# Kernel optimization log

Measured on AMD Instinct MI355X. Metric: run time of the kernel, lower is better.

The kernel has to match this reference:

```python
import jax, jax.numpy as jnp
import numpy as np
from jax import lax

SIGMA = 1.0
NUM_ITER = 6
NEG = -1e4  # log-domain 'impossible' (fp16-safe)
S = 4       # trellis states (memory-2 RSC)

# RSC code, generators (7,5) octal: feedback 1+D+D^2, feedforward 1+D^2.
# state s = 2*s1 + s2 (s1 = newest register).
_NS = np.zeros((S, 2), np.int32)   # next state per (state, input bit)
_PAR = np.zeros((S, 2), np.int32)  # parity bit per (state, input bit)
for _s in range(S):
    _s1, _s2 = _s >> 1, _s & 1
    for _u in (0, 1):
        _a = _u ^ _s1 ^ _s2          # feedback bit
        _NS[_s, _u] = (_a << 1) | _s1
        _PAR[_s, _u] = _a ^ _s2
NS = jnp.asarray(_NS)                      # [S,2]
NS_FLAT = jnp.asarray(_NS.reshape(-1))     # [S*2], branch i = s*2+u
PAR_FLAT = jnp.asarray(_PAR.reshape(-1))
PAR_BPSK = jnp.asarray(2.0 * _PAR - 1.0, jnp.float32)  # [S,2]
U_BPSK = jnp.asarray([-1.0, 1.0], jnp.float32)


def rsc_encode(bits):
    # bits: [B,K] int32 -> parity bits [B,K] int32 (trellis scan from state 0)
    B = bits.shape[0]
    def step(state, u):
        idx = state * 2 + u
        return NS_FLAT[idx], PAR_FLAT[idx]
    _, p = lax.scan(step, jnp.zeros((B,), jnp.int32), bits.T)
    return p.T


def bcjr(y_sys, y_par, La, Lc):
    # max-log-MAP BCJR. y_sys, y_par, La: [B,T] -> full LLR [B,T]
    B, T = y_sys.shape
    # branch metrics gamma[b,t,s,u]
    gamma = 0.5 * ((Lc * y_sys + La)[:, :, None, None] * U_BPSK
                   + (Lc * y_par)[:, :, None, None] * PAR_BPSK)  # [B,T,S,2]
    gamma_t = jnp.moveaxis(gamma, 1, 0)  # [T,B,S,2]

    # forward recursion (alpha), start in state 0
    alpha0 = jnp.full((B, S), NEG, y_sys.dtype).at[:, 0].set(0.0)
    def fwd(alpha, g):
        cand = (alpha[:, :, None] + g).reshape(B, S * 2)          # [B,8]
        new = jax.ops.segment_max(cand.T, NS_FLAT, num_segments=S).T  # [B,S]
        new = new - new.max(axis=1, keepdims=True)
        return new, alpha                                          # emit alpha_t (pre-step)
    _, alphas = lax.scan(fwd, alpha0, gamma_t)                     # [T,B,S]

    # backward recursion (beta), unterminated trellis -> uniform end
    beta_end = jnp.zeros((B, S), y_sys.dtype)
    def bwd(beta, g):
        new = (g + beta[:, NS]).max(axis=2)                        # [B,S]
        new = new - new.max(axis=1, keepdims=True)
        return new, beta                                           # emit beta_{t+1}
    _, betas = lax.scan(bwd, beta_end, gamma_t, reverse=True)      # [T,B,S]

    metric = alphas[:, :, :, None] + gamma_t + betas[:, :, NS]     # [T,B,S,2]
    llr = metric[..., 1].max(axis=2) - metric[..., 0].max(axis=2)  # [T,B]
    return llr.T


def _turbo(x, n1, n2, n3, interleaver):
    # encode: rate-1/3 turbo (systematic + 2 RSC parities), BPSK, AWGN
    c1 = 2.0 * x.astype(jnp.float32) - 1.0
    c2 = 2.0 * rsc_encode(x).astype(jnp.float32) - 1.0
    xi = jnp.take(x, interleaver, axis=1)
    c3 = 2.0 * rsc_encode(xi).astype(jnp.float32) - 1.0
    y1 = c1 + SIGMA * n1
    y2 = c2 + SIGMA * n2
    y1i = jnp.take(y1, interleaver, axis=1)
    y3 = c3 + SIGMA * n3

    inv = jnp.argsort(interleaver)
    Lc = 2.0 / (SIGMA * SIGMA)
    L_int = jnp.zeros_like(y1)
    L2 = L_int
    for _ in range(NUM_ITER):
        L1 = bcjr(y1, y2, L_int, Lc)
        Le1 = L1 - Lc * y1 - L_int            # extrinsic of decoder 1
        Le1_i = jnp.take(Le1, interleaver, axis=1)
        L2 = bcjr(y1i, y3, Le1_i, Lc)
        Le2 = L2 - Lc * y1i - Le1_i           # extrinsic of decoder 2
        L_int = jnp.take(Le2, inv, axis=1)    # deinterleave
    return jnp.take(L2, inv, axis=1)          # final deinterleaved LLR logits [B,K]


def setup_inputs() -> dict:
    key = jax.random.key(0)
    k1, k2, k3, k4, k5 = jax.random.split(key, 5)
    B, K = 512, 2048
    x = jax.random.randint(k1, (B, K), 0, 2).astype(jnp.int32)
    n1 = jax.random.normal(k2, (B, K), jnp.float32)
    n2 = jax.random.normal(k3, (B, K), jnp.float32)
    n3 = jax.random.normal(k4, (B, K), jnp.float32)
    interleaver = jax.random.permutation(k5, K).astype(jnp.int32)
    return {"x": x, "n1": n1, "n2": n2, "n3": n3, "interleaver": interleaver}


def reference(x, n1, n2, n3, interleaver):
    return _turbo(x, n1, n2, n3, interleaver)
```

## Files before the change

kernel.cpp:

```cpp
#include <hip/hip_runtime.h>

#define KLEN 2048
#define SCH 8
#define TPR 256
#define NEGV (-1e4f)

struct SM {
  float y1[KLEN];
  float y1i[KLEN];
  float Lint[KLEN];
  float A[KLEN];
  unsigned short perm[KLEN];
  unsigned short invp[KLEN];
  float fT[4][16];
  float bT[4][16];
  unsigned int eT[4][2];
};

template <int CTRL>
__device__ __forceinline__ float dppf(float src) {
  return __int_as_float(__builtin_amdgcn_update_dpp(
      __float_as_int(src), __float_as_int(src), CTRL, 0xF, 0xF, false));
}

template <int CTRL>
__device__ __forceinline__ void shift16(const float (&X)[16], float (&T)[16]) {
#pragma unroll
  for (int e = 0; e < 16; ++e) T[e] = dppf<CTRL>(X[e]);
}

__device__ __forceinline__ void cp16(float (&D)[16], const float (&S)[16]) {
#pragma unroll
  for (int e = 0; e < 16; ++e) D[e] = S[e];
}

__device__ __forceinline__ void ld16(float (&D)[16], const float* S) {
#pragma unroll
  for (int e = 0; e < 16; ++e) D[e] = S[e];
}

__device__ __forceinline__ void comb(const float (&X)[16], const float (&Y)[16],
                                     float (&Z)[16]) {
#pragma unroll
  for (int i = 0; i < 4; ++i)
#pragma unroll
    for (int j = 0; j < 4; ++j)
      Z[i * 4 + j] = fmaxf(fmaxf(X[i * 4 + 0] + Y[0 * 4 + j], X[i * 4 + 1] + Y[1 * 4 + j]),
                           fmaxf(X[i * 4 + 2] + Y[2 * 4 + j], X[i * 4 + 3] + Y[3 * 4 + j]));
}

__device__ __forceinline__ void buildM(const float (&p)[SCH], const float (&q)[SCH],
                                       float (&M)[16]) {
  float ppq = p[0] + q[0], pmq = p[0] - q[0];
  M[0] = -ppq; M[1] =  ppq; M[2] = NEGV; M[3] = NEGV;
  M[4] = NEGV; M[5] = NEGV; M[6] =  pmq; M[7] = -pmq;
  M[8] =  ppq; M[9] = -ppq; M[10] = NEGV; M[11] = NEGV;
  M[12] = NEGV; M[13] = NEGV; M[14] = -pmq; M[15] =  pmq;
#pragma unroll
  for (int k = 1; k < SCH; ++k) {
    ppq = p[k] + q[k]; pmq = p[k] - q[k];
#pragma unroll
    for (int j = 0; j < 4; ++j) {
      float r0 = M[0 * 4 + j], r1 = M[1 * 4 + j], r2 = M[2 * 4 + j], r3 = M[3 * 4 + j];
      M[0 * 4 + j] = fmaxf(r0 - ppq, r1 + ppq);
      M[2 * 4 + j] = fmaxf(r0 + ppq, r1 - ppq);
      M[1 * 4 + j] = fmaxf(r2 + pmq, r3 - pmq);
      M[3 * 4 + j] = fmaxf(r2 - pmq, r3 + pmq);
    }
  }
  float mx = M[0];
#pragma unroll
  for (int e = 1; e < 16; ++e) mx = fmaxf(mx, M[e]);
#pragma unroll
  for (int e = 0; e < 16; ++e) M[e] -= mx;
}

__device__ __forceinline__ void bcjr_pass(
    const float* ys, const float* La, float* dst, const unsigned short* widx,
    int finalLLR, const float (&q)[SCH], float (&fT)[4][16], float (&bT)[4][16],
    int c, int lane, int w) {
  const int base = c * SCH;
  float p[SCH];
  {
    const float4* y4 = (const float4*)(ys + base);
    const float4* l4 = (const float4*)(La + base);
#pragma unroll
    for (int k = 0; k < SCH / 4; ++k) {
      float4 yv = y4[k], lv = l4[k];
      p[4 * k + 0] = yv.x + 0.5f * lv.x;
      p[4 * k + 1] = yv.y + 0.5f * lv.y;
      p[4 * k + 2] = yv.z + 0.5f * lv.z;
      p[4 * k + 3] = yv.w + 0.5f * lv.w;
    }
  }

  float P[16];
  buildM(p, q, P);
  float Q[16];
  cp16(Q, P);

  const int rl = lane & 15;
  const int row = lane >> 4;

  {
    float T[16], N[16];
    shift16<0x111>(P, T); if (rl >= 1) { comb(P, T, N); cp16(P, N); }
    shift16<0x112>(P, T); if (rl >= 2) { comb(P, T, N); cp16(P, N); }
    shift16<0x114>(P, T); if (rl >= 4) { comb(P, T, N); cp16(P, N); }
    shift16<0x118>(P, T); if (rl >= 8) { comb(P, T, N); cp16(P, N); }
    shift16<0x142>(P, T); if (row & 1)  { comb(P, T, N); cp16(P, N); }
    shift16<0x143>(P, T); if (row >= 2) { comb(P, T, N); cp16(P, N); }
  }
  {
    float T[16], N[16];
    shift16<0x101>(Q, T); if (rl <= 14) { comb(T, Q, N); cp16(Q, N); }
    shift16<0x102>(Q, T); if (rl <= 13) { comb(T, Q, N); cp16(Q, N); }
    shift16<0x104>(Q, T); if (rl <= 11) { comb(T, Q, N); cp16(Q, N); }
    shift16<0x108>(Q, T); if (rl <= 7)  { comb(T, Q, N); cp16(Q, N); }
#pragma unroll
    for (int d = 1; d <= 2; d <<= 1) {
      int src = (row + d) << 4;
      float T2[16];
#pragma unroll
      for (int e = 0; e < 16; ++e) T2[e] = __shfl(Q[e], src);
      if (row + d <= 3) { float N2[16]; comb(T2, Q, N2); cp16(Q, N2); }
    }
  }

  if (lane == 63) {
#pragma unroll
    for (int e = 0; e < 16; ++e) fT[w][e] = P[e];
  }
  if (lane == 0) {
#pragma unroll
    for (int e = 0; e < 16; ++e) bT[w][e] = Q[e];
  }
  __syncthreads();

  float F[16];
  {
    float t[16], n[16];
    if (w >= 1) ld16(F, fT[0]);
    if (w >= 2) { ld16(t, fT[1]); comb(t, F, n); cp16(F, n); }
    if (w >= 3) { ld16(t, fT[2]); comb(t, F, n); cp16(F, n); }
    if (w >= 1) { comb(P, F, n); cp16(P, n); }
  }
  float Bm[16];
  {
    float t[16], n[16];
    if (w <= 2) ld16(Bm, bT[3]);
    if (w <= 1) { ld16(t, bT[2]); comb(Bm, t, n); cp16(Bm, n); }
    if (w <= 0) { ld16(t, bT[1]); comb(Bm, t, n); cp16(Bm, n); }
    if (w <= 2) { comb(Bm, Q, n); cp16(Q, n); }
  }

  float a[4];
  {
    float a0 = __shfl(P[0], lane - 1), a1 = __shfl(P[4], lane - 1);
    float a2 = __shfl(P[8], lane - 1), a3 = __shfl(P[12], lane - 1);
    if (c == 0) { a[0] = 0.f; a[1] = NEGV; a[2] = NEGV; a[3] = NEGV; }
    else {
      if (lane == 0) { a0 = F[0]; a1 = F[4]; a2 = F[8]; a3 = F[12]; }
      a[0] = 0.f; a[1] = a1 - a0; a[2] = a2 - a0; a[3] = a3 - a0;
    }
  }

  float b[4];
  {
    float m0 = fmaxf(fmaxf(Q[0], Q[4]), fmaxf(Q[8],  Q[12]));
    float m1 = fmaxf(fmaxf(Q[1], Q[5]), fmaxf(Q[9],  Q[13]));
    float m2 = fmaxf(fmaxf(Q[2], Q[6]), fmaxf(Q[10], Q[14]));
    float m3 = fmaxf(fmaxf(Q[3], Q[7]), fmaxf(Q[11], Q[15]));
    float b0 = __shfl(m0, lane + 1), b1 = __shfl(m1, lane + 1);
    float b2 = __shfl(m2, lane + 1), b3 = __shfl(m3, lane + 1);
    if (c == TPR - 1) { b[0] = b[1] = b[2] = b[3] = 0.f; }
    else {
      if (lane == 63) {
        b0 = fmaxf(fmaxf(Bm[0], Bm[4]), fmaxf(Bm[8],  Bm[12]));
        b1 = fmaxf(fmaxf(Bm[1], Bm[5]), fmaxf(Bm[9],  Bm[13]));
        b2 = fmaxf(fmaxf(Bm[2], Bm[6]), fmaxf(Bm[10], Bm[14]));
        b3 = fmaxf(fmaxf(Bm[3], Bm[7]), fmaxf(Bm[11], Bm[15]));
      }
      b[0] = 0.f; b[1] = b1 - b0; b[2] = b2 - b0; b[3] = b3 - b0;
    }
  }

  float bet[SCH][4];
  bet[SCH - 1][0] = b[0]; bet[SCH - 1][1] = b[1];
  bet[SCH - 1][2] = b[2]; bet[SCH - 1][3] = b[3];
#pragma unroll
  for (int k = SCH - 1; k >= 1; --k) {
    float ppq = p[k] + q[k], pmq = p[k] - q[k];
    float B0 = bet[k][0], B1 = bet[k][1], B2 = bet[k][2], B3 = bet[k][3];
    bet[k - 1][0] = fmaxf(B0 - ppq, B2 + ppq);
    bet[k - 1][1] = fmaxf(B2 - ppq, B0 + ppq);
    bet[k - 1][2] = fmaxf(B3 - pmq, B1 + pmq);
    bet[k - 1][3] = fmaxf(B1 - pmq, B3 + pmq);
  }

#pragma unroll
  for (int k = 0; k < SCH; ++k) {
    float ppq = p[k] + q[k], pmq = p[k] - q[k];
    float B0 = bet[k][0], B1 = bet[k][1], B2 = bet[k][2], B3 = bet[k][3];
    float m1 = fmaxf(fmaxf(a[0] + ppq + B2, a[1] + ppq + B0),
                     fmaxf(a[2] + pmq + B1, a[3] + pmq + B3));
    float m0 = fmaxf(fmaxf(a[0] - ppq + B0, a[1] - ppq + B2),
                     fmaxf(a[2] - pmq + B3, a[3] - pmq + B1));
    float llr = m1 - m0;
    float val = finalLLR ? llr : (llr - 2.f * p[k]);
    dst[widx[base + k]] = val;
    float a0 = a[0], a1 = a[1], a2 = a[2], a3 = a[3];
    a[0] = fmaxf(a0 - ppq, a1 + ppq);
    a[2] = fmaxf(a0 + ppq, a1 - ppq);
    a[1] = fmaxf(a2 + pmq, a3 - pmq);
    a[3] = fmaxf(a2 - pmq, a3 + pmq);
  }
}

__device__ __forceinline__ unsigned fsm_compose(unsigned f, unsigned g) {
  unsigned nm = 0;
#pragma unroll
  for (int s = 0; s < 4; ++s) {
    unsigned gs = (g >> (8 * s)) & 3u;
    nm |= ((f >> (8 * gs)) & 0xFFu) << (8 * s);
  }
  return nm;
}

__global__ __launch_bounds__(TPR, 2) void turbo_kernel(
    const int* __restrict__ xg, const float* __restrict__ n1g,
    const float* __restrict__ n2g, const float* __restrict__ n3g,
    const int* __restrict__ pg, float* __restrict__ outg) {
  __shared__ SM sm;
  const int tid = threadIdx.x;
  const int c = tid, lane = tid & 63, w = tid >> 6;
  const size_t rb = (size_t)blockIdx.x * KLEN;

  int* Ai = (int*)sm.A;
  for (int i = tid; i < KLEN; i += TPR) {
    sm.perm[i] = (unsigned short)pg[i];
    int xv = xg[rb + i];
    Ai[i] = xv;
    sm.y1[i] = (2.f * xv - 1.f) + n1g[rb + i];
    sm.Lint[i] = 0.f;
  }
  float q2[SCH], q3[SCH];
  {
    size_t g0 = rb + (size_t)c * SCH;
#pragma unroll
    for (int k = 0; k < SCH; ++k) { q2[k] = n2g[g0 + k]; q3[k] = n3g[g0 + k]; }
  }
  __syncthreads();

  for (int i = tid; i < KLEN; i += TPR) {
    sm.invp[sm.perm[i]] = (unsigned short)i;
    sm.y1i[i] = sm.y1[sm.perm[i]];
  }

  unsigned ub1 = 0, ub2 = 0;
#pragma unroll
  for (int k = 0; k < SCH; ++k) {
    int t = c * SCH + k;
    ub1 |= (unsigned)(Ai[t] & 1) << k;
    ub2 |= (unsigned)(Ai[sm.perm[t]] & 1) << k;
  }
  unsigned m1 = 0x03020100u, m2 = 0x03020100u;
#pragma unroll
  for (int k = 0; k < SCH; ++k) {
    unsigned st1 = ((ub1 >> k) & 1) ? 0x03010002u : 0x01030200u;
    unsigned st2 = ((ub2 >> k) & 1) ? 0x03010002u : 0x01030200u;
    m1 = fsm_compose(st1, m1);
    m2 = fsm_compose(st2, m2);
  }
#pragma unroll
  for (int i = 0; i < 6; ++i) {
    const int d = 1 << i;
    unsigned t1 = __shfl_up(m1, d), t2 = __shfl_up(m2, d);
    if (lane >= d) { m1 = fsm_compose(m1, t1); m2 = fsm_compose(m2, t2); }
  }
  if (lane == 63) { sm.eT[w][0] = m1; sm.eT[w][1] = m2; }
  __syncthreads();
  {
    unsigned W1 = 0x03020100u, W2 = 0x03020100u;
    if (w >= 1) { W1 = sm.eT[0][0]; W2 = sm.eT[0][1]; }
    if (w >= 2) { W1 = fsm_compose(sm.eT[1][0], W1); W2 = fsm_compose(sm.eT[1][1], W2); }
    if (w >= 3) { W1 = fsm_compose(sm.eT[2][0], W1); W2 = fsm_compose(sm.eT[2][1], W2); }
    unsigned f1 = fsm_compose(m1, W1), f2 = fsm_compose(m2, W2);
    unsigned pf1 = __shfl_up(f1, 1), pf2 = __shfl_up(f2, 1);
    int s1 = (c == 0) ? 0 : (lane == 0 ? (int)(W1 & 3u) : (int)(pf1 & 3u));
    int s2 = (c == 0) ? 0 : (lane == 0 ? (int)(W2 & 3u) : (int)(pf2 & 3u));
#pragma unroll
    for (int k = 0; k < SCH; ++k) {
      { int u = (ub1 >> k) & 1, a = u ^ (s1 >> 1) ^ (s1 & 1), par = a ^ (s1 & 1);
        q2[k] += 2.f * par - 1.f; s1 = (a << 1) | (s1 >> 1); }
      { int u = (ub2 >> k) & 1, a = u ^ (s2 >> 1) ^ (s2 & 1), par = a ^ (s2 & 1);
        q3[k] += 2.f * par - 1.f; s2 = (a << 1) | (s2 >> 1); }
    }
  }
  __syncthreads();

#pragma unroll 1
  for (int it = 0; it < 6; ++it) {
    bcjr_pass(sm.y1, sm.Lint, sm.A, sm.invp, 0, q2, sm.fT, sm.bT, c, lane, w);
    __syncthreads();
    const int fin = (it == 5);
    bcjr_pass(sm.y1i, sm.A, sm.Lint, sm.perm, fin, q3, sm.fT, sm.bT, c, lane, w);
    __syncthreads();
  }

  for (int i = tid; i < KLEN; i += TPR) outg[rb + i] = sm.Lint[i];
}

extern "C" void kernel_launch(void* const* d_in, const int* in_sizes, int n_in,
                              void* d_out, int out_size, void* d_ws, size_t ws_size,
                              hipStream_t stream) {
  (void)n_in; (void)d_ws; (void)ws_size; (void)out_size;
  const int* x    = (const int*)d_in[0];
  const float* n1 = (const float*)d_in[1];
  const float* n2 = (const float*)d_in[2];
  const float* n3 = (const float*)d_in[3];
  const int* perm = (const int*)d_in[4];
  float* out = (float*)d_out;
  const int K = in_sizes[4];
  const int B = in_sizes[0] / K;
  turbo_kernel<<<B, TPR, 0, stream>>>(x, n1, n2, n3, perm, out);
}
```

Baseline: 174.7 us.

## Use packed fp32 adds with reordered 4x4 matrix layout in BCJR scans

Reorders the 4x4 max-plus transition matrices and the alpha/beta state vectors into pairs of float2 and computes the additions with inline-asm v_pk_add_f32 using op_sel broadcasts. The goal is to roughly halve the VALU add instructions in the parallel prefix combines, in matrix construction and in the per-step alpha/beta recursions. The max operations stay scalar, and the inline asm may constrain register allocation and scheduling. DPP and shuffle counts are unchanged.

```diff
diff --git a/kernel.cpp b/kernel.cpp
--- a/kernel.cpp
+++ b/kernel.cpp
@@ -4,6 +4,24 @@
 #define SCH 8
 #define TPR 256
 #define NEGV (-1e4f)
+
+typedef float v2f __attribute__((ext_vector_type(2)));
+
+static __device__ __forceinline__ v2f pka(v2f a, v2f b) {
+  v2f d; asm("v_pk_add_f32 %0, %1, %2" : "=v"(d) : "v"(a), "v"(b)); return d;
+}
+static __device__ __forceinline__ v2f pkabl(v2f a, v2f b) {
+  v2f d; asm("v_pk_add_f32 %0, %1, %2 op_sel:[0,0] op_sel_hi:[1,0]"
+             : "=v"(d) : "v"(a), "v"(b)); return d;
+}
+static __device__ __forceinline__ v2f pkabh(v2f a, v2f b) {
+  v2f d; asm("v_pk_add_f32 %0, %1, %2 op_sel:[0,1] op_sel_hi:[1,1]"
+             : "=v"(d) : "v"(a), "v"(b)); return d;
+}
+static __device__ __forceinline__ v2f pkasw(v2f a, v2f b) {
+  v2f d; asm("v_pk_add_f32 %0, %1, %2 op_sel:[0,1] op_sel_hi:[1,0]"
+             : "=v"(d) : "v"(a), "v"(b)); return d;
+}
 
 struct SM {
   float y1[KLEN];
@@ -12,72 +30,89 @@
   float A[KLEN];
   unsigned short perm[KLEN];
   unsigned short invp[KLEN];
-  float fT[4][16];
-  float bT[4][16];
+  v2f fT[4][8];
+  v2f bT[4][8];
   unsigned int eT[4][2];
 };
 
+
 template <int CTRL>
-__device__ __forceinline__ float dppf(float src) {
-  return __int_as_float(__builtin_amdgcn_update_dpp(
-      __float_as_int(src), __float_as_int(src), CTRL, 0xF, 0xF, false));
+__device__ __forceinline__ v2f dpp2(v2f x) {
+  int lo = __builtin_amdgcn_update_dpp(__float_as_int(x.x), __float_as_int(x.x),
+                                       CTRL, 0xF, 0xF, false);
+  int hi = __builtin_amdgcn_update_dpp(__float_as_int(x.y), __float_as_int(x.y),
+                                       CTRL, 0xF, 0xF, false);
+  v2f r; r.x = __int_as_float(lo); r.y = __int_as_float(hi); return r;
 }
 
 template <int CTRL>
-__device__ __forceinline__ void shift16(const float (&X)[16], float (&T)[16]) {
-#pragma unroll
-  for (int e = 0; e < 16; ++e) T[e] = dppf<CTRL>(X[e]);
-}
-
-__device__ __forceinline__ void cp16(float (&D)[16], const float (&S)[16]) {
-#pragma unroll
-  for (int e = 0; e < 16; ++e) D[e] = S[e];
-}
-
-__device__ __forceinline__ void ld16(float (&D)[16], const float* S) {
-#pragma unroll
-  for (int e = 0; e < 16; ++e) D[e] = S[e];
-}
-
-__device__ __forceinline__ void comb(const float (&X)[16], const float (&Y)[16],
-                                     float (&Z)[16]) {
-#pragma unroll
-  for (int i = 0; i < 4; ++i)
-#pragma unroll
-    for (int j = 0; j < 4; ++j)
-      Z[i * 4 + j] = fmaxf(fmaxf(X[i * 4 + 0] + Y[0 * 4 + j], X[i * 4 + 1] + Y[1 * 4 + j]),
-                           fmaxf(X[i * 4 + 2] + Y[2 * 4 + j], X[i * 4 + 3] + Y[3 * 4 + j]));
+__device__ __forceinline__ void shift8(const v2f (&X)[8], v2f (&T)[8]) {
+#pragma unroll
+  for (int e = 0; e < 8; ++e) T[e] = dpp2<CTRL>(X[e]);
+}
+
+__device__ __forceinline__ void cp8(v2f (&D)[8], const v2f (&S)[8]) {
+#pragma unroll
+  for (int e = 0; e < 8; ++e) D[e] = S[e];
+}
+
+__device__ __forceinline__ void comb(const v2f (&X)[8], const v2f (&Y)[8],
+                                     v2f (&Z)[8]) {
+#pragma unroll
+  for (int j = 0; j < 4; ++j) {
+    v2f y01 = Y[2 * j], y23 = Y[2 * j + 1];
+    v2f a0 = pkabl(X[0], y01), b0 = pkabl(X[1], y01);
+    v2f a1 = pkabh(X[2], y01), b1 = pkabh(X[3], y01);
+    v2f a2 = pkabl(X[4], y23), b2 = pkabl(X[5], y23);
+    v2f a3 = pkabh(X[6], y23), b3 = pkabh(X[7], y23);
+    v2f z01, z23;
+    z01.x = fmaxf(fmaxf(a0.x, a1.x), fmaxf(a2.x, a3.x));
+    z01.y = fmaxf(fmaxf(a0.y, a1.y), fmaxf(a2.y, a3.y));
+    z23.x = fmaxf(fmaxf(b0.x, b1.x), fmaxf(b2.x, b3.x));
+    z23.y = fmaxf(fmaxf(b0.y, b1.y), fmaxf(b2.y, b3.y));
+    Z[2 * j] = z01; Z[2 * j + 1] = z23;
+  }
 }
 
 __device__ __forceinline__ void buildM(const float (&p)[SCH], const float (&q)[SCH],
-                                       float (&M)[16]) {
-  float ppq = p[0] + q[0], pmq = p[0] - q[0];
-  M[0] = -ppq; M[1] =  ppq; M[2] = NEGV; M[3] = NEGV;
-  M[4] = NEGV; M[5] = NEGV; M[6] =  pmq; M[7] = -pmq;
-  M[8] =  ppq; M[9] = -ppq; M[10] = NEGV; M[11] = NEGV;
-  M[12] = NEGV; M[13] = NEGV; M[14] = -pmq; M[15] =  pmq;
+                                       v2f (&X)[8]) {
+  {
+    float ppq = p[0] + q[0], pmq = p[0] - q[0];
+    X[0].x = -ppq; X[0].y = NEGV;  X[1].x =  ppq; X[1].y = NEGV;
+    X[2].x =  ppq; X[2].y = NEGV;  X[3].x = -ppq; X[3].y = NEGV;
+    X[4].x = NEGV; X[4].y =  pmq;  X[5].x = NEGV; X[5].y = -pmq;
+    X[6].x = NEGV; X[6].y = -pmq;  X[7].x = NEGV; X[7].y =  pmq;
+  }
 #pragma unroll
   for (int k = 1; k < SCH; ++k) {
-    ppq = p[k] + q[k]; pmq = p[k] - q[k];
+    float ppq = p[k] + q[k], pmq = p[k] - q[k];
+    v2f Wp; Wp.x = -ppq; Wp.y = ppq;
+    v2f Wm; Wm.x = pmq;  Wm.y = -pmq;
 #pragma unroll
     for (int j = 0; j < 4; ++j) {
-      float r0 = M[0 * 4 + j], r1 = M[1 * 4 + j], r2 = M[2 * 4 + j], r3 = M[3 * 4 + j];
-      M[0 * 4 + j] = fmaxf(r0 - ppq, r1 + ppq);
-      M[2 * 4 + j] = fmaxf(r0 + ppq, r1 - ppq);
-      M[1 * 4 + j] = fmaxf(r2 + pmq, r3 - pmq);
-      M[3 * 4 + j] = fmaxf(r2 - pmq, r3 + pmq);
-    }
-  }
-  float mx = M[0];
-#pragma unroll
-  for (int e = 1; e < 16; ++e) mx = fmaxf(mx, M[e]);
-#pragma unroll
-  for (int e = 0; e < 16; ++e) M[e] -= mx;
+      v2f c01 = X[2 * j], c23 = X[2 * j + 1];
+      v2f t = pka(c01, Wp);
+      v2f u = pkasw(c01, Wp);
+      v2f v = pka(c23, Wm);
+      v2f s = pkasw(c23, Wm);
+      v2f n01, n23;
+      n01.x = fmaxf(t.x, t.y); n01.y = fmaxf(v.x, v.y);
+      n23.x = fmaxf(u.x, u.y); n23.y = fmaxf(s.x, s.y);
+      X[2 * j] = n01; X[2 * j + 1] = n23;
+    }
+  }
+  float mx = fmaxf(fmaxf(fmaxf(X[0].x, X[0].y), fmaxf(X[1].x, X[1].y)),
+                   fmaxf(fmaxf(X[2].x, X[2].y), fmaxf(X[3].x, X[3].y)));
+  mx = fmaxf(mx, fmaxf(fmaxf(fmaxf(X[4].x, X[4].y), fmaxf(X[5].x, X[5].y)),
+                       fmaxf(fmaxf(X[6].x, X[6].y), fmaxf(X[7].x, X[7].y))));
+  v2f mn; mn.x = -mx; mn.y = -mx;
+#pragma unroll
+  for (int e = 0; e < 8; ++e) X[e] = pka(X[e], mn);
 }
 
 __device__ __forceinline__ void bcjr_pass(
     const float* ys, const float* La, float* dst, const unsigned short* widx,
-    int finalLLR, const float (&q)[SCH], float (&fT)[4][16], float (&bT)[4][16],
+    int finalLLR, const float (&q)[SCH], v2f (&fT)[4][8], v2f (&bT)[4][8],
     int c, int lane, int w) {
   const int base = c * SCH;
   float p[SCH];
@@ -94,126 +129,129 @@
     }
   }
 
-  float P[16];
+  v2f P[8];
   buildM(p, q, P);
-  float Q[16];
-  cp16(Q, P);
+  v2f Q[8];
+  cp8(Q, P);
 
   const int rl = lane & 15;
   const int row = lane >> 4;
 
   {
-    float T[16], N[16];
-    shift16<0x111>(P, T); if (rl >= 1) { comb(P, T, N); cp16(P, N); }
-    shift16<0x112>(P, T); if (rl >= 2) { comb(P, T, N); cp16(P, N); }
-    shift16<0x114>(P, T); if (rl >= 4) { comb(P, T, N); cp16(P, N); }
-    shift16<0x118>(P, T); if (rl >= 8) { comb(P, T, N); cp16(P, N); }
-    shift16<0x142>(P, T); if (row & 1)  { comb(P, T, N); cp16(P, N); }
-    shift16<0x143>(P, T); if (row >= 2) { comb(P, T, N); cp16(P, N); }
-  }
-  {
-    float T[16], N[16];
-    shift16<0x101>(Q, T); if (rl <= 14) { comb(T, Q, N); cp16(Q, N); }
-    shift16<0x102>(Q, T); if (rl <= 13) { comb(T, Q, N); cp16(Q, N); }
-    shift16<0x104>(Q, T); if (rl <= 11) { comb(T, Q, N); cp16(Q, N); }
-    shift16<0x108>(Q, T); if (rl <= 7)  { comb(T, Q, N); cp16(Q, N); }
+    v2f T[8], N[8];
+    shift8<0x111>(P, T); if (rl >= 1) { comb(P, T, N); cp8(P, N); }
+    shift8<0x112>(P, T); if (rl >= 2) { comb(P, T, N); cp8(P, N); }
+    shift8<0x114>(P, T); if (rl >= 4) { comb(P, T, N); cp8(P, N); }
+    shift8<0x118>(P, T); if (rl >= 8) { comb(P, T, N); cp8(P, N); }
+    shift8<0x142>(P, T); if (row & 1)  { comb(P, T, N); cp8(P, N); }
+    shift8<0x143>(P, T); if (row >= 2) { comb(P, T, N); cp8(P, N); }
+  }
+  {
+    v2f T[8], N[8];
+    shift8<0x101>(Q, T); if (rl <= 14) { comb(T, Q, N); cp8(Q, N); }
+    shift8<0x102>(Q, T); if (rl <= 13) { comb(T, Q, N); cp8(Q, N); }
+    shift8<0x104>(Q, T); if (rl <= 11) { comb(T, Q, N); cp8(Q, N); }
+    shift8<0x108>(Q, T); if (rl <= 7)  { comb(T, Q, N); cp8(Q, N); }
 #pragma unroll
     for (int d = 1; d <= 2; d <<= 1) {
       int src = (row + d) << 4;
-      float T2[16];
-#pragma unroll
-      for (int e = 0; e < 16; ++e) T2[e] = __shfl(Q[e], src);
-      if (row + d <= 3) { float N2[16]; comb(T2, Q, N2); cp16(Q, N2); }
-    }
-  }
-
-  if (lane == 63) {
-#pragma unroll
-    for (int e = 0; e < 16; ++e) fT[w][e] = P[e];
-  }
-  if (lane == 0) {
-#pragma unroll
-    for (int e = 0; e < 16; ++e) bT[w][e] = Q[e];
-  }
+      v2f T2[8];
+#pragma unroll
+      for (int e = 0; e < 8; ++e) {
+        T2[e].x = __shfl(Q[e].x, src);
+        T2[e].y = __shfl(Q[e].y, src);
+      }
+      if (row + d <= 3) { v2f N2[8]; comb(T2, Q, N2); cp8(Q, N2); }
+    }
+  }
+
+  if (lane == 63) cp8(fT[w], P);
+  if (lane == 0)  cp8(bT[w], Q);
   __syncthreads();
 
-  float F[16];
-  {
-    float t[16], n[16];
-    if (w >= 1) ld16(F, fT[0]);
-    if (w >= 2) { ld16(t, fT[1]); comb(t, F, n); cp16(F, n); }
-    if (w >= 3) { ld16(t, fT[2]); comb(t, F, n); cp16(F, n); }
-    if (w >= 1) { comb(P, F, n); cp16(P, n); }
-  }
-  float Bm[16];
-  {
-    float t[16], n[16];
-    if (w <= 2) ld16(Bm, bT[3]);
-    if (w <= 1) { ld16(t, bT[2]); comb(Bm, t, n); cp16(Bm, n); }
-    if (w <= 0) { ld16(t, bT[1]); comb(Bm, t, n); cp16(Bm, n); }
-    if (w <= 2) { comb(Bm, Q, n); cp16(Q, n); }
-  }
-
-  float a[4];
-  {
-    float a0 = __shfl(P[0], lane - 1), a1 = __shfl(P[4], lane - 1);
-    float a2 = __shfl(P[8], lane - 1), a3 = __shfl(P[12], lane - 1);
-    if (c == 0) { a[0] = 0.f; a[1] = NEGV; a[2] = NEGV; a[3] = NEGV; }
+  v2f F[8];
+  {
+    v2f t[8], n[8];
+    if (w >= 1) cp8(F, fT[0]);
+    if (w >= 2) { cp8(t, fT[1]); comb(t, F, n); cp8(F, n); }
+    if (w >= 3) { cp8(t, fT[2]); comb(t, F, n); cp8(F, n); }
+    if (w >= 1) { comb(P, F, n); cp8(P, n); }
+  }
+  v2f Bm[8];
+  {
+    v2f t[8], n[8];
+    if (w <= 2) cp8(Bm, bT[3]);
+    if (w <= 1) { cp8(t, bT[2]); comb(Bm, t, n); cp8(Bm, n); }
+    if (w <= 0) { cp8(t, bT[1]); comb(Bm, t, n); cp8(Bm, n); }
+    if (w <= 2) { comb(Bm, Q, n); cp8(Q, n); }
+  }
+
+  v2f A01, A23;
+  {
+    float a0 = __shfl(P[0].x, lane - 1), a1 = __shfl(P[0].y, lane - 1);
+    float a2 = __shfl(P[1].x, lane - 1), a3 = __shfl(P[1].y, lane - 1);
+    if (c == 0) { A01.x = 0.f; A01.y = NEGV; A23.x = NEGV; A23.y = NEGV; }
     else {
-      if (lane == 0) { a0 = F[0]; a1 = F[4]; a2 = F[8]; a3 = F[12]; }
-      a[0] = 0.f; a[1] = a1 - a0; a[2] = a2 - a0; a[3] = a3 - a0;
-    }
-  }
-
-  float b[4];
-  {
-    float m0 = fmaxf(fmaxf(Q[0], Q[4]), fmaxf(Q[8],  Q[12]));
-    float m1 = fmaxf(fmaxf(Q[1], Q[5]), fmaxf(Q[9],  Q[13]));
-    float m2 = fmaxf(fmaxf(Q[2], Q[6]), fmaxf(Q[10], Q[14]));
-    float m3 = fmaxf(fmaxf(Q[3], Q[7]), fmaxf(Q[11], Q[15]));
+      if (lane == 0) { a0 = F[0].x; a1 = F[0].y; a2 = F[1].x; a3 = F[1].y; }
+      A01.x = 0.f; A01.y = a1 - a0; A23.x = a2 - a0; A23.y = a3 - a0;
+    }
+  }
+
+  v2f B02, B13;
+  {
+    float m0 = fmaxf(fmaxf(Q[0].x, Q[0].y), fmaxf(Q[1].x, Q[1].y));
+    float m1 = fmaxf(fmaxf(Q[2].x, Q[2].y), fmaxf(Q[3].x, Q[3].y));
+    float m2 = fmaxf(fmaxf(Q[4].x, Q[4].y), fmaxf(Q[5].x, Q[5].y));
+    float m3 = fmaxf(fmaxf(Q[6].x, Q[6].y), fmaxf(Q[7].x, Q[7].y));
     float b0 = __shfl(m0, lane + 1), b1 = __shfl(m1, lane + 1);
     float b2 = __shfl(m2, lane + 1), b3 = __shfl(m3, lane + 1);
-    if (c == TPR - 1) { b[0] = b[1] = b[2] = b[3] = 0.f; }
+    if (c == TPR - 1) { B02.x = 0.f; B02.y = 0.f; B13.x = 0.f; B13.y = 0.f; }
     else {
       if (lane == 63) {
-        b0 = fmaxf(fmaxf(Bm[0], Bm[4]), fmaxf(Bm[8],  Bm[12]));
-        b1 = fmaxf(fmaxf(Bm[1], Bm[5]), fmaxf(Bm[9],  Bm[13]));
-        b2 = fmaxf(fmaxf(Bm[2], Bm[6]), fmaxf(Bm[10], Bm[14]));
-        b3 = fmaxf(fmaxf(Bm[3], Bm[7]), fmaxf(Bm[11], Bm[15]));
+        b0 = fmaxf(fmaxf(Bm[0].x, Bm[0].y), fmaxf(Bm[1].x, Bm[1].y));
+        b1 = fmaxf(fmaxf(Bm[2].x, Bm[2].y), fmaxf(Bm[3].x, Bm[3].y));
+        b2 = fmaxf(fmaxf(Bm[4].x, Bm[4].y), fmaxf(Bm[5].x, Bm[5].y));
+        b3 = fmaxf(fmaxf(Bm[6].x, Bm[6].y), fmaxf(Bm[7].x, Bm[7].y));
       }
-      b[0] = 0.f; b[1] = b1 - b0; b[2] = b2 - b0; b[3] = b3 - b0;
-    }
-  }
-
-  float bet[SCH][4];
-  bet[SCH - 1][0] = b[0]; bet[SCH - 1][1] = b[1];
-  bet[SCH - 1][2] = b[2]; bet[SCH - 1][3] = b[3];
+      B02.x = 0.f; B02.y = b2 - b0; B13.x = b1 - b0; B13.y = b3 - b0;
+    }
+  }
+
+  v2f bet02[SCH], bet13[SCH];
+  bet02[SCH - 1] = B02; bet13[SCH - 1] = B13;
 #pragma unroll
   for (int k = SCH - 1; k >= 1; --k) {
     float ppq = p[k] + q[k], pmq = p[k] - q[k];
-    float B0 = bet[k][0], B1 = bet[k][1], B2 = bet[k][2], B3 = bet[k][3];
-    bet[k - 1][0] = fmaxf(B0 - ppq, B2 + ppq);
-    bet[k - 1][1] = fmaxf(B2 - ppq, B0 + ppq);
-    bet[k - 1][2] = fmaxf(B3 - pmq, B1 + pmq);
-    bet[k - 1][3] = fmaxf(B1 - pmq, B3 + pmq);
+    v2f Wp; Wp.x = -ppq; Wp.y = ppq;
+    v2f Wm; Wm.x = pmq;  Wm.y = -pmq;
+    v2f P02 = bet02[k], P13 = bet13[k];
+    v2f t = pka(P02, Wp);
+    v2f u = pkasw(P02, Wp);
+    v2f v = pka(P13, Wm);
+    v2f s = pkasw(P13, Wm);
+    v2f n02, n13;
+    n02.x = fmaxf(t.x, t.y);  n02.y = fmaxf(v.x, v.y);
+    n13.x = fmaxf(u.x, u.y);  n13.y = fmaxf(s.x, s.y);
+    bet02[k - 1] = n02; bet13[k - 1] = n13;
   }
 
 #pragma unroll
   for (int k = 0; k < SCH; ++k) {
     float ppq = p[k] + q[k], pmq = p[k] - q[k];
-    float B0 = bet[k][0], B1 = bet[k][1], B2 = bet[k][2], B3 = bet[k][3];
-    float m1 = fmaxf(fmaxf(a[0] + ppq + B2, a[1] + ppq + B0),
-                     fmaxf(a[2] + pmq + B1, a[3] + pmq + B3));
-    float m0 = fmaxf(fmaxf(a[0] - ppq + B0, a[1] - ppq + B2),
-                     fmaxf(a[2] - pmq + B3, a[3] - pmq + B1));
+    v2f Wp; Wp.x = -ppq; Wp.y = ppq;
+    v2f Wm; Wm.x = pmq;  Wm.y = -pmq;
+    v2f t = pka(A01, Wp);
+    v2f u = pkasw(A01, Wp);
+    v2f v = pka(A23, Wm);
+    v2f s = pkasw(A23, Wm);
+    float B0 = bet02[k].x, B2 = bet02[k].y, B1 = bet13[k].x, B3 = bet13[k].y;
+    float m1 = fmaxf(fmaxf(t.y + B0, u.x + B2), fmaxf(v.x + B1, s.y + B3));
+    float m0 = fmaxf(fmaxf(t.x + B0, u.y + B2), fmaxf(s.x + B3, v.y + B1));
     float llr = m1 - m0;
     float val = finalLLR ? llr : (llr - 2.f * p[k]);
     dst[widx[base + k]] = val;
-    float a0 = a[0], a1 = a[1], a2 = a[2], a3 = a[3];
-    a[0] = fmaxf(a0 - ppq, a1 + ppq);
-    a[2] = fmaxf(a0 + ppq, a1 - ppq);
-    a[1] = fmaxf(a2 + pmq, a3 - pmq);
-    a[3] = fmaxf(a2 - pmq, a3 + pmq);
+    A01.x = fmaxf(t.x, t.y);  A01.y = fmaxf(v.x, v.y);
+    A23.x = fmaxf(u.x, u.y);  A23.y = fmaxf(s.x, s.y);
   }
 }
 
```

Measured after the change: 202.0 us. +15.7%, slower.

## Replace matrix-matrix cross-wave combines with vector-matrix products in BCJR scan

Applied to the files above, without the earlier changes.

Forward and backward boundary states are now propagated as 4-element vectors times 4x4 max-plus matrices instead of full 16-element matrix-matrix compositions. The backward suffix across waves reuses the forward total matrices stored in shared memory, so the separate backward shared table and its write are dropped. The two cross-row shuffle-combine steps on Q are replaced by vector-matrix updates. This cuts max-plus arithmetic, register pressure and LDS traffic per pass, at the cost of three serial row shuffles of 16 values each.

```diff
diff --git a/kernel.cpp b/kernel.cpp
--- a/kernel.cpp
+++ b/kernel.cpp
@@ -13,7 +13,6 @@
   unsigned short perm[KLEN];
   unsigned short invp[KLEN];
   float fT[4][16];
-  float bT[4][16];
   unsigned int eT[4][2];
 };
 
@@ -34,11 +33,6 @@
   for (int e = 0; e < 16; ++e) D[e] = S[e];
 }
 
-__device__ __forceinline__ void ld16(float (&D)[16], const float* S) {
-#pragma unroll
-  for (int e = 0; e < 16; ++e) D[e] = S[e];
-}
-
 __device__ __forceinline__ void comb(const float (&X)[16], const float (&Y)[16],
                                      float (&Z)[16]) {
 #pragma unroll
@@ -47,6 +41,22 @@
     for (int j = 0; j < 4; ++j)
       Z[i * 4 + j] = fmaxf(fmaxf(X[i * 4 + 0] + Y[0 * 4 + j], X[i * 4 + 1] + Y[1 * 4 + j]),
                            fmaxf(X[i * 4 + 2] + Y[2 * 4 + j], X[i * 4 + 3] + Y[3 * 4 + j]));
+}
+
+__device__ __forceinline__ void matcol(const float* T, float (&f)[4]) {
+  float r0 = fmaxf(fmaxf(T[0]  + f[0], T[1]  + f[1]), fmaxf(T[2]  + f[2], T[3]  + f[3]));
+  float r1 = fmaxf(fmaxf(T[4]  + f[0], T[5]  + f[1]), fmaxf(T[6]  + f[2], T[7]  + f[3]));
+  float r2 = fmaxf(fmaxf(T[8]  + f[0], T[9]  + f[1]), fmaxf(T[10] + f[2], T[11] + f[3]));
+  float r3 = fmaxf(fmaxf(T[12] + f[0], T[13] + f[1]), fmaxf(T[14] + f[2], T[15] + f[3]));
+  f[0] = r0; f[1] = r1; f[2] = r2; f[3] = r3;
+}
+
+__device__ __forceinline__ void rowmat(float (&u)[4], const float* T) {
+  float c0 = fmaxf(fmaxf(u[0] + T[0], u[1] + T[4]), fmaxf(u[2] + T[8],  u[3] + T[12]));
+  float c1 = fmaxf(fmaxf(u[0] + T[1], u[1] + T[5]), fmaxf(u[2] + T[9],  u[3] + T[13]));
+  float c2 = fmaxf(fmaxf(u[0] + T[2], u[1] + T[6]), fmaxf(u[2] + T[10], u[3] + T[14]));
+  float c3 = fmaxf(fmaxf(u[0] + T[3], u[1] + T[7]), fmaxf(u[2] + T[11], u[3] + T[15]));
+  u[0] = c0; u[1] = c1; u[2] = c2; u[3] = c3;
 }
 
 __device__ __forceinline__ void buildM(const float (&p)[SCH], const float (&q)[SCH],
@@ -77,7 +87,7 @@
 
 __device__ __forceinline__ void bcjr_pass(
     const float* ys, const float* La, float* dst, const unsigned short* widx,
-    int finalLLR, const float (&q)[SCH], float (&fT)[4][16], float (&bT)[4][16],
+    int finalLLR, const float (&q)[SCH], float (&fT)[4][16],
     int c, int lane, int w) {
   const int base = c * SCH;
   float p[SCH];
@@ -117,72 +127,58 @@
     shift16<0x102>(Q, T); if (rl <= 13) { comb(T, Q, N); cp16(Q, N); }
     shift16<0x104>(Q, T); if (rl <= 11) { comb(T, Q, N); cp16(Q, N); }
     shift16<0x108>(Q, T); if (rl <= 7)  { comb(T, Q, N); cp16(Q, N); }
-#pragma unroll
-    for (int d = 1; d <= 2; d <<= 1) {
-      int src = (row + d) << 4;
-      float T2[16];
-#pragma unroll
-      for (int e = 0; e < 16; ++e) T2[e] = __shfl(Q[e], src);
-      if (row + d <= 3) { float N2[16]; comb(T2, Q, N2); cp16(Q, N2); }
-    }
-  }
-
-  if (lane == 63) {
-#pragma unroll
-    for (int e = 0; e < 16; ++e) fT[w][e] = P[e];
-  }
-  if (lane == 0) {
-#pragma unroll
-    for (int e = 0; e < 16; ++e) bT[w][e] = Q[e];
-  }
+  }
+
+  if (lane == 63) cp16(fT[w], P);
   __syncthreads();
 
-  float F[16];
-  {
-    float t[16], n[16];
-    if (w >= 1) ld16(F, fT[0]);
-    if (w >= 2) { ld16(t, fT[1]); comb(t, F, n); cp16(F, n); }
-    if (w >= 3) { ld16(t, fT[2]); comb(t, F, n); cp16(F, n); }
-    if (w >= 1) { comb(P, F, n); cp16(P, n); }
-  }
-  float Bm[16];
-  {
-    float t[16], n[16];
-    if (w <= 2) ld16(Bm, bT[3]);
-    if (w <= 1) { ld16(t, bT[2]); comb(Bm, t, n); cp16(Bm, n); }
-    if (w <= 0) { ld16(t, bT[1]); comb(Bm, t, n); cp16(Bm, n); }
-    if (w <= 2) { comb(Bm, Q, n); cp16(Q, n); }
+  float f[4];
+  if (w == 0) { f[0] = 0.f; f[1] = NEGV; f[2] = NEGV; f[3] = NEGV; }
+  else {
+    f[0] = fT[0][0]; f[1] = fT[0][4]; f[2] = fT[0][8]; f[3] = fT[0][12];
+    if (w >= 2) matcol(fT[1], f);
+    if (w >= 3) matcol(fT[2], f);
+  }
+  float u[4];
+  if (w == 3) { u[0] = u[1] = u[2] = u[3] = 0.f; }
+  else {
+    const float* T3 = fT[3];
+#pragma unroll
+    for (int j = 0; j < 4; ++j)
+      u[j] = fmaxf(fmaxf(T3[j], T3[4 + j]), fmaxf(T3[8 + j], T3[12 + j]));
+    if (w <= 1) rowmat(u, fT[2]);
+    if (w == 0) rowmat(u, fT[1]);
+  }
+#pragma unroll
+  for (int jj = 3; jj >= 1; --jj) {
+    float T[16];
+#pragma unroll
+    for (int e = 0; e < 16; ++e) T[e] = __shfl(Q[e], jj << 4);
+    if (row < jj) rowmat(u, T);
   }
 
   float a[4];
   {
-    float a0 = __shfl(P[0], lane - 1), a1 = __shfl(P[4], lane - 1);
-    float a2 = __shfl(P[8], lane - 1), a3 = __shfl(P[12], lane - 1);
-    if (c == 0) { a[0] = 0.f; a[1] = NEGV; a[2] = NEGV; a[3] = NEGV; }
-    else {
-      if (lane == 0) { a0 = F[0]; a1 = F[4]; a2 = F[8]; a3 = F[12]; }
-      a[0] = 0.f; a[1] = a1 - a0; a[2] = a2 - a0; a[3] = a3 - a0;
-    }
+    float v0 = fmaxf(fmaxf(P[0]  + f[0], P[1]  + f[1]), fmaxf(P[2]  + f[2], P[3]  + f[3]));
+    float v1 = fmaxf(fmaxf(P[4]  + f[0], P[5]  + f[1]), fmaxf(P[6]  + f[2], P[7]  + f[3]));
+    float v2 = fmaxf(fmaxf(P[8]  + f[0], P[9]  + f[1]), fmaxf(P[10] + f[2], P[11] + f[3]));
+    float v3 = fmaxf(fmaxf(P[12] + f[0], P[13] + f[1]), fmaxf(P[14] + f[2], P[15] + f[3]));
+    float a0 = __shfl(v0, lane - 1), a1 = __shfl(v1, lane - 1);
+    float a2 = __shfl(v2, lane - 1), a3 = __shfl(v3, lane - 1);
+    if (lane == 0) { a0 = f[0]; a1 = f[1]; a2 = f[2]; a3 = f[3]; }
+    a[0] = 0.f; a[1] = a1 - a0; a[2] = a2 - a0; a[3] = a3 - a0;
   }
 
   float b[4];
   {
-    float m0 = fmaxf(fmaxf(Q[0], Q[4]), fmaxf(Q[8],  Q[12]));
-    float m1 = fmaxf(fmaxf(Q[1], Q[5]), fmaxf(Q[9],  Q[13]));
-    float m2 = fmaxf(fmaxf(Q[2], Q[6]), fmaxf(Q[10], Q[14]));
-    float m3 = fmaxf(fmaxf(Q[3], Q[7]), fmaxf(Q[11], Q[15]));
-    float b0 = __shfl(m0, lane + 1), b1 = __shfl(m1, lane + 1);
-    float b2 = __shfl(m2, lane + 1), b3 = __shfl(m3, lane + 1);
-    if (c == TPR - 1) { b[0] = b[1] = b[2] = b[3] = 0.f; }
-    else {
-      if (lane == 63) {
-        b0 = fmaxf(fmaxf(Bm[0], Bm[4]), fmaxf(Bm[8],  Bm[12]));
-        b1 = fmaxf(fmaxf(Bm[1], Bm[5]), fmaxf(Bm[9],  Bm[13]));
-        b2 = fmaxf(fmaxf(Bm[2], Bm[6]), fmaxf(Bm[10], Bm[14]));
-        b3 = fmaxf(fmaxf(Bm[3], Bm[7]), fmaxf(Bm[11], Bm[15]));
-      }
-      b[0] = 0.f; b[1] = b1 - b0; b[2] = b2 - b0; b[3] = b3 - b0;
-    }
+    float z0 = fmaxf(fmaxf(u[0] + Q[0], u[1] + Q[4]), fmaxf(u[2] + Q[8],  u[3] + Q[12]));
+    float z1 = fmaxf(fmaxf(u[0] + Q[1], u[1] + Q[5]), fmaxf(u[2] + Q[9],  u[3] + Q[13]));
+    float z2 = fmaxf(fmaxf(u[0] + Q[2], u[1] + Q[6]), fmaxf(u[2] + Q[10], u[3] + Q[14]));
+    float z3 = fmaxf(fmaxf(u[0] + Q[3], u[1] + Q[7]), fmaxf(u[2] + Q[11], u[3] + Q[15]));
+    float b0 = __shfl(z0, lane + 1), b1 = __shfl(z1, lane + 1);
+    float b2 = __shfl(z2, lane + 1), b3 = __shfl(z3, lane + 1);
+    if (lane == 63) { b0 = u[0]; b1 = u[1]; b2 = u[2]; b3 = u[3]; }
+    b[0] = 0.f; b[1] = b1 - b0; b[2] = b2 - b0; b[3] = b3 - b0;
   }
 
   float bet[SCH][4];
@@ -301,10 +297,10 @@
 
 #pragma unroll 1
   for (int it = 0; it < 6; ++it) {
-    bcjr_pass(sm.y1, sm.Lint, sm.A, sm.invp, 0, q2, sm.fT, sm.bT, c, lane, w);
+    bcjr_pass(sm.y1, sm.Lint, sm.A, sm.invp, 0, q2, sm.fT, c, lane, w);
     __syncthreads();
     const int fin = (it == 5);
-    bcjr_pass(sm.y1i, sm.A, sm.Lint, sm.perm, fin, q3, sm.fT, sm.bT, c, lane, w);
+    bcjr_pass(sm.y1i, sm.A, sm.Lint, sm.perm, fin, q3, sm.fT, c, lane, w);
     __syncthreads();
   }
 
```

Result: faster. 165.4 us (-5.3%).
